# Kernel tuning notes

Hardware: AMD Instinct MI355X
Metric: run time of the kernel (lower is better)

## Reference

```python
import jax, jax.numpy as jnp
import numpy as np

N_VERTS = 50000
N_FACES = 100000
D_IN = 256
D_OUT = 256


def setup_inputs() -> dict:
    key = jax.random.key(0)
    k1, k2, k3, k4 = jax.random.split(key, 4)
    shape_features = jax.random.normal(k1, (N_VERTS, D_IN), dtype=jnp.float32)
    faces = jax.random.randint(k2, (N_FACES, 3), 0, N_VERTS, dtype=jnp.int64)
    scale = 1.0 / np.sqrt(D_IN)
    W1 = jax.random.normal(k3, (D_OUT, D_IN), dtype=jnp.float32) * scale
    b1 = jnp.zeros((D_OUT,), dtype=jnp.float32)
    W2 = jax.random.normal(k4, (D_OUT, D_IN), dtype=jnp.float32) * scale
    b2 = jnp.zeros((D_OUT,), dtype=jnp.float32)
    return {"shape_features": shape_features, "faces": faces,
            "W1": W1, "b1": b1, "W2": W2, "b2": b2}


def reference(shape_features, faces, W1, b1, W2, b2):
    # out = linear1(x) + linear2(sum over neighbors of x)
    # Each triangle face (i1,i2,i3) makes every pair mutual neighbors.
    n_verts = shape_features.shape[0]
    i1, i2, i3 = faces[:, 0], faces[:, 1], faces[:, 2]
    # receiver (segment id) and neighbor (gather source) for 6 directed pairs/face
    recv = jnp.concatenate([i1, i1, i2, i2, i3, i3])
    nbr = jnp.concatenate([i2, i3, i1, i3, i1, i2])
    # ragged neighbor gather-sum as one segment_sum  [E, D] -> [V, D]
    aggr = jax.ops.segment_sum(shape_features[nbr], recv, num_segments=n_verts)
    out = (shape_features @ W1.T + b1) + (aggr @ W2.T + b2)
    return out
```

## Files before the change

### kernel.cpp

```cpp
#include <hip/hip_runtime.h>
#include <hip/hip_bf16.h>

typedef float f32x4 __attribute__((ext_vector_type(4)));
typedef int   i32x4 __attribute__((ext_vector_type(4)));

#define NV   50000
#define PADM 50048
#define NF   100000
#define CAP  32
#define QSCALE (5.0f / 127.0f)
#define QINV   (127.0f / 5.0f)
#define WSCALE (0.35f / 127.0f)
#define WINV   (127.0f / 0.35f)

__device__ __forceinline__ void load_lds16(const void* g, void* lds) {
    __builtin_amdgcn_global_load_lds(
        (const __attribute__((address_space(1))) unsigned int*)g,
        (__attribute__((address_space(3))) unsigned int*)lds,
        16, 0, 0);
}

__device__ __forceinline__ int q8(float x) {
    float c = fminf(fmaxf(x * QINV, -127.0f), 127.0f);
    return __float2int_rn(c);
}
__device__ __forceinline__ int qw8(float x) {
    float c = fminf(fmaxf(x * WINV, -127.0f), 127.0f);
    return __float2int_rn(c);
}

__global__ __launch_bounds__(256) void convert_kernel(
    const float* __restrict__ f, const float* __restrict__ W1, const float* __restrict__ W2,
    unsigned char* __restrict__ fQ, unsigned char* __restrict__ wQ1,
    unsigned char* __restrict__ wQ2, unsigned* __restrict__ cursor)
{
    const int CQ = PADM * 64;
    const int CW = 16384;
    int gid = blockIdx.x * 256 + threadIdx.x;
    if (gid < NV) cursor[gid] = 0u;
    int stride = gridDim.x * 256;
    for (int i = gid; i < CQ + 2 * CW; i += stride) {
        if (i < CQ) {
            int row = i >> 6;
            f32x4 v = {};
            if (row < NV) v = *reinterpret_cast<const f32x4*>(f + (size_t)i * 4);
            unsigned pq = (unsigned)(q8(v[0]) & 255) | ((unsigned)(q8(v[1]) & 255) << 8)
                        | ((unsigned)(q8(v[2]) & 255) << 16) | ((unsigned)(q8(v[3]) & 255) << 24);
            *reinterpret_cast<unsigned*>(fQ + (size_t)i * 4) = pq;
        } else {
            int j = (i - CQ) % CW;
            const float* Wsrc = (i - CQ < CW) ? W1 : W2;
            unsigned char* Wdst = (i - CQ < CW) ? wQ1 : wQ2;
            f32x4 v = *reinterpret_cast<const f32x4*>(Wsrc + (size_t)j * 4);
            unsigned pq = (unsigned)(qw8(v[0]) & 255) | ((unsigned)(qw8(v[1]) & 255) << 8)
                        | ((unsigned)(qw8(v[2]) & 255) << 16) | ((unsigned)(qw8(v[3]) & 255) << 24);
            *reinterpret_cast<unsigned*>(Wdst + (size_t)j * 4) = pq;
        }
    }
}

__global__ __launch_bounds__(256) void fill_kernel(const int* __restrict__ faces,
                                                   unsigned* __restrict__ cursor,
                                                   unsigned* __restrict__ entries) {
    int i = blockIdx.x * 256 + threadIdx.x;
    if (i >= 3 * NF) return;
    int fi = i / 3, c = i - fi * 3;
    unsigned v0 = (unsigned)faces[3 * fi + 0];
    unsigned v1 = (unsigned)faces[3 * fi + 1];
    unsigned v2 = (unsigned)faces[3 * fi + 2];
    unsigned me = (c == 0) ? v0 : (c == 1) ? v1 : v2;
    unsigned na = (c == 0) ? v1 : v0;
    unsigned nb = (c == 2) ? v1 : v2;
    unsigned s = atomicAdd(&cursor[me], 1u);
    if (s < CAP) entries[me * CAP + s] = (na << 16) | nb;
}

__device__ __forceinline__ void add8(int* acc, uint2 r) {
    #pragma unroll
    for (int j = 0; j < 4; ++j) {
        acc[j]     += (int)((signed char)(r.x >> (j * 8)));
        acc[4 + j] += (int)((signed char)(r.y >> (j * 8)));
    }
}

__global__ __launch_bounds__(256) void aggr_kernel(const unsigned* __restrict__ cursor,
                                                   const unsigned* __restrict__ entries,
                                                   const unsigned char* __restrict__ fQ,
                                                   unsigned char* __restrict__ aggrQ,
                                                   float* __restrict__ rsA) {
    int v = blockIdx.x * 4 + (threadIdx.x >> 6);
    if (v >= NV) return;
    const int l    = threadIdx.x & 63;
    const int half = l >> 5;
    const int q    = (l & 31) << 3;
    unsigned cnt = cursor[v];
    if (cnt > CAP) cnt = CAP;
    const unsigned* eb = entries + (size_t)v * CAP;

    int acc[8] = {};
    unsigned e = half;
    for (; e + 2 < cnt; e += 4) {
        unsigned p0 = eb[e], p1 = eb[e + 2];
        uint2 r0 = *reinterpret_cast<const uint2*>(fQ + (size_t)(p0 >> 16)    * 256 + q);
        uint2 r1 = *reinterpret_cast<const uint2*>(fQ + (size_t)(p0 & 0xffff) * 256 + q);
        uint2 r2 = *reinterpret_cast<const uint2*>(fQ + (size_t)(p1 >> 16)    * 256 + q);
        uint2 r3 = *reinterpret_cast<const uint2*>(fQ + (size_t)(p1 & 0xffff) * 256 + q);
        add8(acc, r0); add8(acc, r1); add8(acc, r2); add8(acc, r3);
    }
    if (e < cnt) {
        unsigned p0 = eb[e];
        uint2 r0 = *reinterpret_cast<const uint2*>(fQ + (size_t)(p0 >> 16)    * 256 + q);
        uint2 r1 = *reinterpret_cast<const uint2*>(fQ + (size_t)(p0 & 0xffff) * 256 + q);
        add8(acc, r0); add8(acc, r1);
    }
    float vals[8];
    float mx = 0.0f;
    #pragma unroll
    for (int j = 0; j < 8; ++j) {
        int tot = acc[j] + __shfl_xor(acc[j], 32, 64);
        vals[j] = (float)tot * QSCALE;
        mx = fmaxf(mx, fabsf(vals[j]));
    }
    #pragma unroll
    for (int s = 1; s < 32; s <<= 1) mx = fmaxf(mx, __shfl_xor(mx, s, 64));
    float inv = (mx > 0.0f) ? (127.0f / mx) : 0.0f;
    unsigned lo = 0, hi = 0;
    #pragma unroll
    for (int j = 0; j < 4; ++j) {
        lo |= ((unsigned)(__float2int_rn(vals[j]     * inv) & 255)) << (j * 8);
        hi |= ((unsigned)(__float2int_rn(vals[4 + j] * inv) & 255)) << (j * 8);
    }
    if (half == 0) {
        uint2 pk = { lo, hi };
        *reinterpret_cast<uint2*>(aggrQ + (size_t)v * 256 + q) = pk;
        if (l == 0) rsA[v] = mx * (1.0f / 127.0f);
    }
}

__global__ __launch_bounds__(512, 4) void gemm_kernel(
    const unsigned char* __restrict__ fQ, const unsigned char* __restrict__ aggrQ,
    const unsigned char* __restrict__ wQ1, const unsigned char* __restrict__ wQ2,
    const float* __restrict__ rsA,
    const float* __restrict__ b1, const float* __restrict__ b2,
    float* __restrict__ out)
{
    __shared__ __align__(16) unsigned char smem[81920];
    const int t  = threadIdx.x;
    const int l  = t & 63;
    const int w  = t >> 6;
    const int wm = w >> 2;
    const int wn = w & 3;
    const int m0 = blockIdx.x * 64;
    const int lr8 = l >> 3;
    const int lc  = l & 7;
    const int gko = ((lc ^ lr8) << 4);

    i32x4 accI1[2][4] = {};
    i32x4 accI2[2][4] = {};

    auto STAGE = [&](int buf, int ti) {
        const unsigned char* Ab = (ti < 2) ? fQ  : aggrQ;
        const unsigned char* Bb = (ti < 2) ? wQ1 : wQ2;
        const int ko = (ti & 1) * 128;
        unsigned char* As = smem + buf * 8192;
        unsigned char* Bs = smem + 16384 + buf * 32768;
        load_lds16(Ab + (size_t)(m0 + w * 8 + lr8) * 256 + ko + gko, As + w * 1024);
        #pragma unroll
        for (int it = 0; it < 4; ++it) {
            int cb = w + it * 8;
            load_lds16(Bb + (size_t)(cb * 8 + lr8) * 256 + ko + gko, Bs + cb * 1024);
        }
    };

    STAGE(0, 0);

    #pragma unroll
    for (int ti = 0; ti < 4; ++ti) {
        const int cur = ti & 1;
        if (ti < 3) {
            STAGE(cur ^ 1, ti + 1);
            asm volatile("s_waitcnt vmcnt(5)" ::: "memory");
        } else {
            asm volatile("s_waitcnt vmcnt(0)" ::: "memory");
        }
        __builtin_amdgcn_s_barrier();

        const unsigned char* As = smem + cur * 8192;
        const unsigned char* Bs = smem + 16384 + cur * 32768;

        i32x4 af[2][2], bf[4][2];
        #pragma unroll
        for (int ks = 0; ks < 2; ++ks) {
            #pragma unroll
            for (int mf = 0; mf < 2; ++mf) {
                int lrow = wm * 32 + mf * 16 + (l & 15);
                int byte = lrow * 128 + ((ks * 64 + (l >> 4) * 16) ^ ((lrow & 7) << 4));
                af[mf][ks] = *reinterpret_cast<const i32x4*>(As + byte);
            }
            #pragma unroll
            for (int nf = 0; nf < 4; ++nf) {
                int lcol = wn * 64 + nf * 16 + (l & 15);
                int byte = lcol * 128 + ((ks * 64 + (l >> 4) * 16) ^ ((lcol & 7) << 4));
                bf[nf][ks] = *reinterpret_cast<const i32x4*>(Bs + byte);
            }
        }
        asm volatile("s_waitcnt lgkmcnt(0)" ::: "memory");
        __builtin_amdgcn_sched_barrier(0);
        __builtin_amdgcn_s_barrier();

        if (ti < 2) {
            #pragma unroll
            for (int ks = 0; ks < 2; ++ks)
                #pragma unroll
                for (int mf = 0; mf < 2; ++mf)
                    #pragma unroll
                    for (int nf = 0; nf < 4; ++nf)
                        accI1[mf][nf] = __builtin_amdgcn_mfma_i32_16x16x64_i8(
                            af[mf][ks], bf[nf][ks], accI1[mf][nf], 0, 0, 0);
        } else {
            #pragma unroll
            for (int ks = 0; ks < 2; ++ks)
                #pragma unroll
                for (int mf = 0; mf < 2; ++mf)
                    #pragma unroll
                    for (int nf = 0; nf < 4; ++nf)
                        accI2[mf][nf] = __builtin_amdgcn_mfma_i32_16x16x64_i8(
                            af[mf][ks], bf[nf][ks], accI2[mf][nf], 0, 0, 0);
        }
    }

    const float S1 = QSCALE * WSCALE;
    float s2[2][4];
    #pragma unroll
    for (int mf = 0; mf < 2; ++mf)
        #pragma unroll
        for (int j = 0; j < 4; ++j)
            s2[mf][j] = rsA[m0 + wm * 32 + mf * 16 + (l >> 4) * 4 + j] * WSCALE;

    __syncthreads();
    float* epi = reinterpret_cast<float*>(smem);
    #pragma unroll
    for (int nf = 0; nf < 4; ++nf) {
        int n = wn * 64 + nf * 16 + (l & 15);
        float bias = b1[n] + b2[n];
        #pragma unroll
        for (int mf = 0; mf < 2; ++mf) {
            #pragma unroll
            for (int j = 0; j < 4; ++j) {
                int rl = wm * 32 + mf * 16 + (l >> 4) * 4 + j;
                epi[rl * 256 + n] = (float)accI1[mf][nf][j] * S1
                                  + (float)accI2[mf][nf][j] * s2[mf][j] + bias;
            }
        }
    }
    __syncthreads();
    #pragma unroll
    for (int it = 0; it < 8; ++it) {
        int chunk = it * 512 + t;
        int row = chunk >> 6;
        int c4  = (chunk & 63) << 2;
        int m = m0 + row;
        if (m < NV)
            *reinterpret_cast<f32x4*>(out + (size_t)m * 256 + c4) =
                *reinterpret_cast<const f32x4*>(epi + (size_t)chunk * 4);
    }
}

extern "C" void kernel_launch(void* const* d_in, const int* in_sizes, int n_in,
                              void* d_out, int out_size, void* d_ws, size_t ws_size,
                              hipStream_t stream)
{
    const float* f     = (const float*)d_in[0];
    const int*   faces = (const int*)d_in[1];
    const float* W1    = (const float*)d_in[2];
    const float* b1    = (const float*)d_in[3];
    const float* W2    = (const float*)d_in[4];
    const float* b2    = (const float*)d_in[5];
    float* out = (float*)d_out;

    char* ws = (char*)d_ws;
    unsigned char* fQ      = (unsigned char*)(ws);
    unsigned char* aggrQ   = (unsigned char*)(ws + 12812288);
    unsigned char* wQ1     = (unsigned char*)(ws + 25624576);
    unsigned char* wQ2     = (unsigned char*)(ws + 25690112);
    float*         rsA     = (float*)(ws + 25755648);
    unsigned*      cursor  = (unsigned*)(ws + 25955840);
    unsigned*      entries = (unsigned*)(ws + 26155840);

    convert_kernel<<<2048, 256, 0, stream>>>(f, W1, W2, fQ, wQ1, wQ2, cursor);
    fill_kernel<<<(3 * NF + 255) / 256, 256, 0, stream>>>(faces, cursor, entries);
    aggr_kernel<<<(NV + 3) / 4, 256, 0, stream>>>(cursor, entries, fQ, aggrQ, rsA);
    gemm_kernel<<<PADM / 64, 512, 0, stream>>>(fQ, aggrQ, wQ1, wQ2, rsA, b1, b2, out);
}
```

Baseline: 82.30 us.

## Fuse neighbor aggregation into GEMM kernel, keeping quantized aggregate in LDS

Moves the per-vertex neighbor gather-sum and requantization into the GEMM kernel. Each block aggregates its 64 rows directly into swizzled LDS along with per-row scales, removing the aggrQ/rsA global round trip and one kernel launch. The A tiles for the own-feature half are loaded once up front, while the B weight tiles become single-buffered and are reloaded between steps with a full vmcnt wait. The cost is less latency hiding in the GEMM and a gather phase that now runs at 782-block, 512-thread granularity, which may cut the occupancy available for the latency-bound gather.

Measured after the change: 93.22 us. 1.13x slower.

```diff
diff --git a/kernel.cpp b/kernel.cpp
--- a/kernel.cpp
+++ b/kernel.cpp
@@ -83,68 +83,19 @@
     }
 }
 
-__global__ __launch_bounds__(256) void aggr_kernel(const unsigned* __restrict__ cursor,
-                                                   const unsigned* __restrict__ entries,
-                                                   const unsigned char* __restrict__ fQ,
-                                                   unsigned char* __restrict__ aggrQ,
-                                                   float* __restrict__ rsA) {
-    int v = blockIdx.x * 4 + (threadIdx.x >> 6);
-    if (v >= NV) return;
-    const int l    = threadIdx.x & 63;
-    const int half = l >> 5;
-    const int q    = (l & 31) << 3;
-    unsigned cnt = cursor[v];
-    if (cnt > CAP) cnt = CAP;
-    const unsigned* eb = entries + (size_t)v * CAP;
-
-    int acc[8] = {};
-    unsigned e = half;
-    for (; e + 2 < cnt; e += 4) {
-        unsigned p0 = eb[e], p1 = eb[e + 2];
-        uint2 r0 = *reinterpret_cast<const uint2*>(fQ + (size_t)(p0 >> 16)    * 256 + q);
-        uint2 r1 = *reinterpret_cast<const uint2*>(fQ + (size_t)(p0 & 0xffff) * 256 + q);
-        uint2 r2 = *reinterpret_cast<const uint2*>(fQ + (size_t)(p1 >> 16)    * 256 + q);
-        uint2 r3 = *reinterpret_cast<const uint2*>(fQ + (size_t)(p1 & 0xffff) * 256 + q);
-        add8(acc, r0); add8(acc, r1); add8(acc, r2); add8(acc, r3);
-    }
-    if (e < cnt) {
-        unsigned p0 = eb[e];
-        uint2 r0 = *reinterpret_cast<const uint2*>(fQ + (size_t)(p0 >> 16)    * 256 + q);
-        uint2 r1 = *reinterpret_cast<const uint2*>(fQ + (size_t)(p0 & 0xffff) * 256 + q);
-        add8(acc, r0); add8(acc, r1);
-    }
-    float vals[8];
-    float mx = 0.0f;
-    #pragma unroll
-    for (int j = 0; j < 8; ++j) {
-        int tot = acc[j] + __shfl_xor(acc[j], 32, 64);
-        vals[j] = (float)tot * QSCALE;
-        mx = fmaxf(mx, fabsf(vals[j]));
-    }
-    #pragma unroll
-    for (int s = 1; s < 32; s <<= 1) mx = fmaxf(mx, __shfl_xor(mx, s, 64));
-    float inv = (mx > 0.0f) ? (127.0f / mx) : 0.0f;
-    unsigned lo = 0, hi = 0;
-    #pragma unroll
-    for (int j = 0; j < 4; ++j) {
-        lo |= ((unsigned)(__float2int_rn(vals[j]     * inv) & 255)) << (j * 8);
-        hi |= ((unsigned)(__float2int_rn(vals[4 + j] * inv) & 255)) << (j * 8);
-    }
-    if (half == 0) {
-        uint2 pk = { lo, hi };
-        *reinterpret_cast<uint2*>(aggrQ + (size_t)v * 256 + q) = pk;
-        if (l == 0) rsA[v] = mx * (1.0f / 127.0f);
-    }
-}
-
-__global__ __launch_bounds__(512, 4) void gemm_kernel(
-    const unsigned char* __restrict__ fQ, const unsigned char* __restrict__ aggrQ,
+__global__ __launch_bounds__(512, 4) void fused_kernel(
+    const unsigned char* __restrict__ fQ,
     const unsigned char* __restrict__ wQ1, const unsigned char* __restrict__ wQ2,
-    const float* __restrict__ rsA,
+    const unsigned* __restrict__ cursor, const unsigned* __restrict__ entries,
     const float* __restrict__ b1, const float* __restrict__ b2,
     float* __restrict__ out)
 {
-    __shared__ __align__(16) unsigned char smem[81920];
+    __shared__ __align__(16) unsigned char smem[65792];
+    unsigned char* Bs   = smem;
+    unsigned char* As01 = smem + 32768;
+    unsigned char* Agg  = smem + 49152;
+    float*         rsL  = reinterpret_cast<float*>(smem + 65536);
+
     const int t  = threadIdx.x;
     const int l  = t & 63;
     const int w  = t >> 6;
@@ -155,38 +106,78 @@
     const int lc  = l & 7;
     const int gko = ((lc ^ lr8) << 4);
 
+    #pragma unroll
+    for (int ti = 0; ti < 2; ++ti)
+        load_lds16(fQ + (size_t)(m0 + w * 8 + lr8) * 256 + ti * 128 + gko,
+                   As01 + ti * 8192 + w * 1024);
+    #pragma unroll
+    for (int it = 0; it < 4; ++it) {
+        int cb = w + it * 8;
+        load_lds16(wQ1 + (size_t)(cb * 8 + lr8) * 256 + gko, Bs + cb * 1024);
+    }
+
+    const int half = l >> 5;
+    const int q    = (l & 31) << 3;
+    for (int it = 0; it < 8; ++it) {
+        int r = w * 8 + it;
+        int v = m0 + r;
+        float vals[8] = {};
+        float mx = 0.0f;
+        if (v < NV) {
+            unsigned cnt = cursor[v];
+            if (cnt > CAP) cnt = CAP;
+            const unsigned* eb = entries + (size_t)v * CAP;
+            int acc[8] = {};
+            unsigned e = half;
+            for (; e + 2 < cnt; e += 4) {
+                unsigned p0 = eb[e], p1 = eb[e + 2];
+                uint2 r0 = *reinterpret_cast<const uint2*>(fQ + (size_t)(p0 >> 16)    * 256 + q);
+                uint2 r1 = *reinterpret_cast<const uint2*>(fQ + (size_t)(p0 & 0xffff) * 256 + q);
+                uint2 r2 = *reinterpret_cast<const uint2*>(fQ + (size_t)(p1 >> 16)    * 256 + q);
+                uint2 r3 = *reinterpret_cast<const uint2*>(fQ + (size_t)(p1 & 0xffff) * 256 + q);
+                add8(acc, r0); add8(acc, r1); add8(acc, r2); add8(acc, r3);
+            }
+            if (e < cnt) {
+                unsigned p0 = eb[e];
+                uint2 r0 = *reinterpret_cast<const uint2*>(fQ + (size_t)(p0 >> 16)    * 256 + q);
+                uint2 r1 = *reinterpret_cast<const uint2*>(fQ + (size_t)(p0 & 0xffff) * 256 + q);
+                add8(acc, r0); add8(acc, r1);
+            }
+            #pragma unroll
+            for (int j = 0; j < 8; ++j) {
+                int tot = acc[j] + __shfl_xor(acc[j], 32, 64);
+                vals[j] = (float)tot * QSCALE;
+                mx = fmaxf(mx, fabsf(vals[j]));
+            }
+            #pragma unroll
+            for (int s = 1; s < 32; s <<= 1) mx = fmaxf(mx, __shfl_xor(mx, s, 64));
+        }
+        float inv = (mx > 0.0f) ? (127.0f / mx) : 0.0f;
+        unsigned lo = 0, hi = 0;
+        #pragma unroll
+        for (int j = 0; j < 4; ++j) {
+            lo |= ((unsigned)(__float2int_rn(vals[j]     * inv) & 255)) << (j * 8);
+            hi |= ((unsigned)(__float2int_rn(vals[4 + j] * inv) & 255)) << (j * 8);
+        }
+        if (half == 0) {
+            int h  = (l >> 4) & 1;
+            int kq = (l & 15) * 8;
+            int byte = h * 8192 + r * 128 + (kq ^ ((r & 7) << 4));
+            uint2 pk = { lo, hi };
+            *reinterpret_cast<uint2*>(Agg + byte) = pk;
+            if (l == 0) rsL[r] = mx * (1.0f / 127.0f);
+        }
+    }
+
+    asm volatile("s_waitcnt lgkmcnt(0) vmcnt(0)" ::: "memory");
+    __builtin_amdgcn_s_barrier();
+
     i32x4 accI1[2][4] = {};
     i32x4 accI2[2][4] = {};
 
-    auto STAGE = [&](int buf, int ti) {
-        const unsigned char* Ab = (ti < 2) ? fQ  : aggrQ;
-        const unsigned char* Bb = (ti < 2) ? wQ1 : wQ2;
-        const int ko = (ti & 1) * 128;
-        unsigned char* As = smem + buf * 8192;
-        unsigned char* Bs = smem + 16384 + buf * 32768;
-        load_lds16(Ab + (size_t)(m0 + w * 8 + lr8) * 256 + ko + gko, As + w * 1024);
-        #pragma unroll
-        for (int it = 0; it < 4; ++it) {
-            int cb = w + it * 8;
-            load_lds16(Bb + (size_t)(cb * 8 + lr8) * 256 + ko + gko, Bs + cb * 1024);
-        }
-    };
-
-    STAGE(0, 0);
-
     #pragma unroll
     for (int ti = 0; ti < 4; ++ti) {
-        const int cur = ti & 1;
-        if (ti < 3) {
-            STAGE(cur ^ 1, ti + 1);
-            asm volatile("s_waitcnt vmcnt(5)" ::: "memory");
-        } else {
-            asm volatile("s_waitcnt vmcnt(0)" ::: "memory");
-        }
-        __builtin_amdgcn_s_barrier();
-
-        const unsigned char* As = smem + cur * 8192;
-        const unsigned char* Bs = smem + 16384 + cur * 32768;
+        const unsigned char* Ab = (ti < 2) ? (As01 + ti * 8192) : (Agg + (ti - 2) * 8192);
 
         i32x4 af[2][2], bf[4][2];
         #pragma unroll
@@ -195,7 +186,7 @@
             for (int mf = 0; mf < 2; ++mf) {
                 int lrow = wm * 32 + mf * 16 + (l & 15);
                 int byte = lrow * 128 + ((ks * 64 + (l >> 4) * 16) ^ ((lrow & 7) << 4));
-                af[mf][ks] = *reinterpret_cast<const i32x4*>(As + byte);
+                af[mf][ks] = *reinterpret_cast<const i32x4*>(Ab + byte);
             }
             #pragma unroll
             for (int nf = 0; nf < 4; ++nf) {
@@ -207,6 +198,16 @@
         asm volatile("s_waitcnt lgkmcnt(0)" ::: "memory");
         __builtin_amdgcn_sched_barrier(0);
         __builtin_amdgcn_s_barrier();
+
+        if (ti < 3) {
+            const unsigned char* Bb = (ti + 1 < 2) ? wQ1 : wQ2;
+            const int ko = ((ti + 1) & 1) * 128;
+            #pragma unroll
+            for (int it = 0; it < 4; ++it) {
+                int cb = w + it * 8;
+                load_lds16(Bb + (size_t)(cb * 8 + lr8) * 256 + ko + gko, Bs + cb * 1024);
+            }
+        }
 
         if (ti < 2) {
             #pragma unroll
@@ -227,6 +228,11 @@
                         accI2[mf][nf] = __builtin_amdgcn_mfma_i32_16x16x64_i8(
                             af[mf][ks], bf[nf][ks], accI2[mf][nf], 0, 0, 0);
         }
+
+        if (ti < 3) {
+            asm volatile("s_waitcnt vmcnt(0)" ::: "memory");
+            __builtin_amdgcn_s_barrier();
+        }
     }
 
     const float S1 = QSCALE * WSCALE;
@@ -235,7 +241,7 @@
     for (int mf = 0; mf < 2; ++mf)
         #pragma unroll
         for (int j = 0; j < 4; ++j)
-            s2[mf][j] = rsA[m0 + wm * 32 + mf * 16 + (l >> 4) * 4 + j] * WSCALE;
+            s2[mf][j] = rsL[wm * 32 + mf * 16 + (l >> 4) * 4 + j] * WSCALE;
 
     __syncthreads();
     float* epi = reinterpret_cast<float*>(smem);
@@ -280,15 +286,12 @@
 
     char* ws = (char*)d_ws;
     unsigned char* fQ      = (unsigned char*)(ws);
-    unsigned char* aggrQ   = (unsigned char*)(ws + 12812288);
-    unsigned char* wQ1     = (unsigned char*)(ws + 25624576);
-    unsigned char* wQ2     = (unsigned char*)(ws + 25690112);
-    float*         rsA     = (float*)(ws + 25755648);
-    unsigned*      cursor  = (unsigned*)(ws + 25955840);
-    unsigned*      entries = (unsigned*)(ws + 26155840);
+    unsigned char* wQ1     = (unsigned char*)(ws + 12812288);
+    unsigned char* wQ2     = (unsigned char*)(ws + 12877824);
+    unsigned*      cursor  = (unsigned*)(ws + 12943360);
+    unsigned*      entries = (unsigned*)(ws + 13143360);
 
     convert_kernel<<<2048, 256, 0, stream>>>(f, W1, W2, fQ, wQ1, wQ2, cursor);
     fill_kernel<<<(3 * NF + 255) / 256, 256, 0, stream>>>(faces, cursor, entries);
-    aggr_kernel<<<(NV + 3) / 4, 256, 0, stream>>>(cursor, entries, fQ, aggrQ, rsA);
-    gemm_kernel<<<PADM / 64, 512, 0, stream>>>(fQ, aggrQ, wQ1, wQ2, rsA, b1, b2, out);
-}
+    fused_kernel<<<PADM / 64, 512, 0, stream>>>(fQ, wQ1, wQ2, cursor, entries, b1, b2, out);
+}
```

## Cut GEMM LDS footprint by single-buffering weights and halving epilogue staging

Applied to the files above, without the earlier changes.

Reduces the GEMM kernel's shared memory from 80KB to 48KB so more blocks fit per CU, and raises the launch-bounds occupancy hint from 4 to 6. The weight (B) tile becomes single-buffered and is reloaded after the fragment reads, while the activation (A) tile stays double-buffered. The epilogue now stages output through LDS in two 32-row halves. The trade-off is an extra full vmcnt wait and barrier each iteration, which exposes the B-load latency, plus more barriers in the epilogue.

Measured after the change: 133.2 us. 61.8% more time.

```diff
diff --git a/kernel.cpp b/kernel.cpp
--- a/kernel.cpp
+++ b/kernel.cpp
@@ -137,14 +137,14 @@
     }
 }
 
-__global__ __launch_bounds__(512, 4) void gemm_kernel(
+__global__ __launch_bounds__(512, 6) void gemm_kernel(
     const unsigned char* __restrict__ fQ, const unsigned char* __restrict__ aggrQ,
     const unsigned char* __restrict__ wQ1, const unsigned char* __restrict__ wQ2,
     const float* __restrict__ rsA,
     const float* __restrict__ b1, const float* __restrict__ b2,
     float* __restrict__ out)
 {
-    __shared__ __align__(16) unsigned char smem[81920];
+    __shared__ __align__(16) unsigned char smem[49152];
     const int t  = threadIdx.x;
     const int l  = t & 63;
     const int w  = t >> 6;
@@ -158,35 +158,34 @@
     i32x4 accI1[2][4] = {};
     i32x4 accI2[2][4] = {};
 
-    auto STAGE = [&](int buf, int ti) {
-        const unsigned char* Ab = (ti < 2) ? fQ  : aggrQ;
+    auto STAGE_A = [&](int buf, int ti) {
+        const unsigned char* Ab = (ti < 2) ? fQ : aggrQ;
+        const int ko = (ti & 1) * 128;
+        load_lds16(Ab + (size_t)(m0 + w * 8 + lr8) * 256 + ko + gko,
+                   smem + 32768 + buf * 8192 + w * 1024);
+    };
+    auto STAGE_B = [&](int ti) {
         const unsigned char* Bb = (ti < 2) ? wQ1 : wQ2;
         const int ko = (ti & 1) * 128;
-        unsigned char* As = smem + buf * 8192;
-        unsigned char* Bs = smem + 16384 + buf * 32768;
-        load_lds16(Ab + (size_t)(m0 + w * 8 + lr8) * 256 + ko + gko, As + w * 1024);
         #pragma unroll
         for (int it = 0; it < 4; ++it) {
             int cb = w + it * 8;
-            load_lds16(Bb + (size_t)(cb * 8 + lr8) * 256 + ko + gko, Bs + cb * 1024);
+            load_lds16(Bb + (size_t)(cb * 8 + lr8) * 256 + ko + gko, smem + cb * 1024);
         }
     };
 
-    STAGE(0, 0);
+    STAGE_A(0, 0);
+    STAGE_B(0);
+    asm volatile("s_waitcnt vmcnt(0)" ::: "memory");
+    __builtin_amdgcn_s_barrier();
 
     #pragma unroll
     for (int ti = 0; ti < 4; ++ti) {
         const int cur = ti & 1;
-        if (ti < 3) {
-            STAGE(cur ^ 1, ti + 1);
-            asm volatile("s_waitcnt vmcnt(5)" ::: "memory");
-        } else {
-            asm volatile("s_waitcnt vmcnt(0)" ::: "memory");
-        }
-        __builtin_amdgcn_s_barrier();
-
-        const unsigned char* As = smem + cur * 8192;
-        const unsigned char* Bs = smem + 16384 + cur * 32768;
+        if (ti < 3) STAGE_A(cur ^ 1, ti + 1);
+
+        const unsigned char* As = smem + 32768 + cur * 8192;
+        const unsigned char* Bs = smem;
 
         i32x4 af[2][2], bf[4][2];
         #pragma unroll
@@ -207,6 +206,7 @@
         asm volatile("s_waitcnt lgkmcnt(0)" ::: "memory");
         __builtin_amdgcn_sched_barrier(0);
         __builtin_amdgcn_s_barrier();
+        if (ti < 3) STAGE_B(ti + 1);
 
         if (ti < 2) {
             #pragma unroll
@@ -227,6 +227,11 @@
                         accI2[mf][nf] = __builtin_amdgcn_mfma_i32_16x16x64_i8(
                             af[mf][ks], bf[nf][ks], accI2[mf][nf], 0, 0, 0);
         }
+
+        if (ti < 3) {
+            asm volatile("s_waitcnt vmcnt(0)" ::: "memory");
+            __builtin_amdgcn_s_barrier();
+        }
     }
 
     const float S1 = QSCALE * WSCALE;
@@ -237,32 +242,37 @@
         for (int j = 0; j < 4; ++j)
             s2[mf][j] = rsA[m0 + wm * 32 + mf * 16 + (l >> 4) * 4 + j] * WSCALE;
 
-    __syncthreads();
     float* epi = reinterpret_cast<float*>(smem);
     #pragma unroll
-    for (int nf = 0; nf < 4; ++nf) {
-        int n = wn * 64 + nf * 16 + (l & 15);
-        float bias = b1[n] + b2[n];
+    for (int h = 0; h < 2; ++h) {
+        __syncthreads();
+        if (wm == h) {
+            #pragma unroll
+            for (int nf = 0; nf < 4; ++nf) {
+                int n = wn * 64 + nf * 16 + (l & 15);
+                float bias = b1[n] + b2[n];
+                #pragma unroll
+                for (int mf = 0; mf < 2; ++mf) {
+                    #pragma unroll
+                    for (int j = 0; j < 4; ++j) {
+                        int r32 = mf * 16 + (l >> 4) * 4 + j;
+                        epi[r32 * 256 + n] = (float)accI1[mf][nf][j] * S1
+                                           + (float)accI2[mf][nf][j] * s2[mf][j] + bias;
+                    }
+                }
+            }
+        }
+        __syncthreads();
         #pragma unroll
-        for (int mf = 0; mf < 2; ++mf) {
-            #pragma unroll
-            for (int j = 0; j < 4; ++j) {
-                int rl = wm * 32 + mf * 16 + (l >> 4) * 4 + j;
-                epi[rl * 256 + n] = (float)accI1[mf][nf][j] * S1
-                                  + (float)accI2[mf][nf][j] * s2[mf][j] + bias;
-            }
-        }
-    }
-    __syncthreads();
-    #pragma unroll
-    for (int it = 0; it < 8; ++it) {
-        int chunk = it * 512 + t;
-        int row = chunk >> 6;
-        int c4  = (chunk & 63) << 2;
-        int m = m0 + row;
-        if (m < NV)
-            *reinterpret_cast<f32x4*>(out + (size_t)m * 256 + c4) =
-                *reinterpret_cast<const f32x4*>(epi + (size_t)chunk * 4);
+        for (int it = 0; it < 4; ++it) {
+            int chunk = it * 512 + t;
+            int row = chunk >> 6;
+            int c4  = (chunk & 63) << 2;
+            int m = m0 + h * 32 + row;
+            if (m < NV)
+                *reinterpret_cast<f32x4*>(out + (size_t)m * 256 + c4) =
+                    *reinterpret_cast<const f32x4*>(epi + (size_t)chunk * 4);
+        }
     }
 }
 
```
